# Optimization experiments

Measured on AMD Instinct MI355X. Metric: run time of the kernel, lower is better.

The kernel has to match this reference:

```python
import jax, jax.numpy as jnp
import numpy as np
import itertools
from functools import partial

H, W = 224, 448            # output raster size
R = 2                      # splat_radius
RADIUS_SCALE = 1.5
B, T, V, GH, GW = 1, 2, 2, 56, 112   # batch, time, views, gaussian grid
N = V * GH * GW            # gaussians per (b,t)
OFFSETS = jnp.array(list(itertools.product(range(-R, R + 1), repeat=2)), dtype=jnp.int32)  # (K,2)


def setup_inputs() -> dict:
    key = jax.random.key(0)
    ks = jax.random.split(key, 8)
    center = jax.random.normal(ks[0], (B, T, V, GH, GW, 3), jnp.float32) * 2.0
    scale = jax.random.uniform(ks[1], (B, T, V, GH, GW, 3), jnp.float32) * 0.1
    feat_dc = jax.random.uniform(ks[2], (B, T, V, GH, GW, 3), jnp.float32)
    opacity = jax.random.uniform(ks[3], (B, T, V, GH, GW, 1), jnp.float32)
    background_prob = jax.random.uniform(ks[4], (B, T, V, GH, GW), jnp.float32)
    sem_proj_2d = jax.random.uniform(ks[5], (B, T, V, 3, H, W), jnp.float32)
    # realistic pinhole intrinsics: fx=fy=220, principal point at image center
    camera_intrinsics = jnp.broadcast_to(jnp.array([220.0, 220.0, W / 2.0, H / 2.0], jnp.float32), (B, V, 4))
    # cameras ~5m behind the (origin-centered) point cloud, identity rotation + jittered translation
    trans = jnp.array([0.0, 0.0, -5.0], jnp.float32) + 0.2 * jax.random.normal(ks[6], (B, T, V, 3), jnp.float32)
    c2w = jnp.broadcast_to(jnp.eye(4, dtype=jnp.float32), (B, T, V, 4, 4))
    camera_to_world = c2w.at[..., :3, 3].set(trans)
    first_ego_pose_world = jnp.broadcast_to(jnp.eye(4, dtype=jnp.float32), (B, 4, 4))
    return {"center": center, "scale": scale, "feat_dc": feat_dc, "opacity": opacity,
            "background_prob": background_prob, "sem_proj_2d": sem_proj_2d,
            "camera_intrinsics": camera_intrinsics, "camera_to_world": camera_to_world,
            "first_ego_pose_world": first_ego_pose_world}


def _render_view(world, scale, color, alpha, intr, c2w):
    # world: (N,4) homogeneous world coords; scale,alpha: (N,); color: (N,3)
    fx, fy, cx, cy = intr[0], intr[1], intr[2], intr[3]
    w2c = jnp.linalg.inv(c2w)
    cam = (world @ w2c.T)[:, :3]              # (N,3) camera-frame coords
    z = cam[:, 2]
    finite = jnp.all(jnp.isfinite(cam), axis=-1)
    valid = (z > 1e-3) & finite & (alpha > 1e-5)
    z_safe = jnp.where(valid, z, 1.0)
    u = cam[:, 0] * fx / z_safe + cx
    v = cam[:, 1] * fy / z_safe + cy
    sigma = jnp.clip((fx + fy) * 0.5 * jnp.abs(scale) / jnp.maximum(z_safe, 1e-3), 0.75, 10.0)
    inb = (u >= -R - 1.0) & (u <= W + R) & (v >= -R - 1.0) & (v <= H + R)
    keep = valid & inb
    cnt = jnp.sum(keep)
    sigma_mean = jnp.where(cnt > 0, jnp.sum(jnp.where(keep, sigma, 0.0)) / jnp.maximum(cnt, 1), 0.0)
    a_eff = jnp.where(keep, alpha, 0.0)
    # depth sort front-to-back; dropped points carry zero alpha so their position is irrelevant
    order = jnp.argsort(jnp.where(keep, z, jnp.inf))
    u_s = jnp.where(keep, u, -1e6)[order]
    v_s = jnp.where(keep, v, -1e6)[order]
    sig_s = sigma[order]
    col_s = color[order]
    a_s = a_eff[order]
    x0 = jnp.floor(u_s).astype(jnp.int32)
    y0 = jnp.floor(v_s).astype(jnp.int32)
    radii = jnp.clip(jnp.ceil(sig_s * RADIUS_SCALE), 1, R).astype(jnp.int32)

    def step(carry, pt):
        alpha_den, rgb_num = carry
        x0p, y0p, up, vp, sp, ap, rp, colp = pt
        xo = x0p + OFFSETS[:, 0]
        yo = y0p + OFFSETS[:, 1]
        keep_off = ((jnp.abs(OFFSETS[:, 0]) <= rp) & (jnp.abs(OFFSETS[:, 1]) <= rp)
                    & (xo >= 0) & (xo < W) & (yo >= 0) & (yo < H))
        sp_c = jnp.maximum(sp, 1e-3)
        du = (up - xo.astype(up.dtype)) / sp_c
        dv = (vp - yo.astype(vp.dtype)) / sp_c
        la = jnp.clip(jnp.exp(-0.5 * (du * du + dv * dv)) * ap, 0.0, 0.999)
        idx = jnp.where(keep_off, yo * W + xo, H * W)   # OOB sentinel -> dropped by scatter
        old = alpha_den[jnp.clip(idx, 0, H * W - 1)]
        transmit = jnp.clip(1.0 - old, 0.0, 1.0)
        contrib = jnp.where(keep_off, la * transmit, 0.0)
        alpha_den = alpha_den.at[idx].set(jnp.clip(old + contrib, 0.0, 0.999), mode='drop')
        rgb_num = rgb_num.at[:, idx].add(colp[:, None] * contrib[None, :], mode='drop')
        return (alpha_den, rgb_num), None

    init = (jnp.zeros(H * W, jnp.float32), jnp.zeros((3, H * W), jnp.float32))
    (alpha_den, rgb_num), _ = jax.lax.scan(step, init, (x0, y0, u_s, v_s, sig_s, a_s, radii, col_s))
    touch = jnp.mean((alpha_den > 1e-6).astype(jnp.float32))
    rgb = jnp.clip(rgb_num, 0.0, 1.0).reshape(3, H, W)
    aout = jnp.clip(alpha_den, 0.0, 1.0).reshape(H, W)
    return rgb, aout, sigma_mean, touch


def _render_branch(centers, scales, colors, alpha, intr, c2w, first_pose):
    cf = centers.reshape(B, T, N, 3)
    sf = jnp.mean(scales, axis=-1).reshape(B, T, N)
    colf = jnp.clip(colors.reshape(B, T, N, 3), 0.0, 1.0)
    af = jnp.clip(alpha.reshape(B, T, N), 0.0, 1.0)
    xyz_h = jnp.concatenate([cf, jnp.ones((B, T, N, 1), cf.dtype)], axis=-1)
    world = jnp.einsum('bij,btnj->btni', first_pose, xyz_h)      # (B,T,N,4)
    M = B * T * V
    wv = jnp.broadcast_to(world[:, :, None], (B, T, V, N, 4)).reshape(M, N, 4)
    sv = jnp.broadcast_to(sf[:, :, None], (B, T, V, N)).reshape(M, N)
    cv = jnp.broadcast_to(colf[:, :, None], (B, T, V, N, 3)).reshape(M, N, 3)
    av = jnp.broadcast_to(af[:, :, None], (B, T, V, N)).reshape(M, N)
    iv = jnp.broadcast_to(intr[:, None], (B, T, V, 4)).reshape(M, 4)
    mv = c2w.reshape(M, 4, 4)
    rgb, aout, sm, tr = jax.vmap(_render_view)(wv, sv, cv, av, iv, mv)
    return (rgb.reshape(B, T, V, 3, H, W), aout.reshape(B, T, V, 1, H, W), jnp.mean(sm), jnp.mean(tr))


def reference(center, scale, feat_dc, opacity, background_prob, sem_proj_2d,
              camera_intrinsics, camera_to_world, first_ego_pose_world):
    base_alpha = jnp.clip(opacity[..., 0], 0.0, 1.0)                      # (B,T,V,GH,GW)
    dyn = jnp.clip(1.0 - background_prob.reshape(B, T, V, GH, GW), 0.0, 1.0)
    a_all = base_alpha
    a_dyn = base_alpha * dyn
    a_sta = base_alpha * (1.0 - dyn)
    rgb_all, al_all, sigma_mean, touch = _render_branch(center, scale, feat_dc, a_all, camera_intrinsics, camera_to_world, first_ego_pose_world)
    rgb_dyn, al_dyn, _, _ = _render_branch(center, scale, feat_dc, a_dyn, camera_intrinsics, camera_to_world, first_ego_pose_world)
    rgb_sta, al_sta, _, _ = _render_branch(center, scale, feat_dc, a_sta, camera_intrinsics, camera_to_world, first_ego_pose_world)
    return (rgb_sta, rgb_dyn, rgb_all, al_sta, al_dyn, al_all, sem_proj_2d, sigma_mean, touch)
```

## Files before the change

### kernel.cpp

```cpp
#include <hip/hip_runtime.h>
#include <cmath>

namespace {
constexpr int Hh = 224, Ww = 448;
constexpr int Tt = 2, Vv = 2, GH = 56, GW = 112;
constexpr int Nn = Vv * GH * GW;
constexpr int TV = Tt * Vv;
constexpr int TOT = TV * Nn;
constexpr int HW = Hh * Ww;
constexpr int TILE = 8;
constexpr int NTX = Ww / TILE;
constexpr int NTY = Hh / TILE;
constexpr int NTILES = TV * NTX * NTY;
constexpr int CAP_T = 256;

constexpr size_t RGB_SZ = (size_t)TV * 3 * HW;
constexpr size_t AL_SZ  = (size_t)TV * HW;
constexpr size_t OFF_RGB_STA = 0;
constexpr size_t OFF_RGB_DYN = RGB_SZ;
constexpr size_t OFF_RGB_ALL = 2 * RGB_SZ;
constexpr size_t OFF_AL_STA  = 3 * RGB_SZ;
constexpr size_t OFF_AL_DYN  = 3 * RGB_SZ + AL_SZ;
constexpr size_t OFF_AL_ALL  = 3 * RGB_SZ + 2 * AL_SZ;
constexpr size_t OFF_SEM     = 3 * RGB_SZ + 3 * AL_SZ;
constexpr size_t OFF_SM      = OFF_SEM + RGB_SZ;
constexpr size_t OFF_TOUCH   = OFF_SM + 1;

constexpr size_t WS_SUM  = (size_t)11 * TOT;
constexpr size_t WS_CNT  = WS_SUM + 4;
constexpr size_t WS_TCNT = WS_CNT + 4;
constexpr size_t WS_TPB  = WS_TCNT + NTILES;
constexpr size_t WS_LIST = WS_TPB + NTILES;
constexpr int    N_ZERO  = 8 + NTILES;
}

__device__ inline unsigned long long shfl_xor_u64(unsigned long long x, int m) {
  unsigned int lo = (unsigned int)x, hi = (unsigned int)(x >> 32);
  lo = __shfl_xor(lo, m, 64);
  hi = __shfl_xor(hi, m, 64);
  return ((unsigned long long)hi << 32) | lo;
}

__global__ __launch_bounds__(256) void init_k(const float4* __restrict__ sem,
                                              float4* __restrict__ dst,
                                              float* __restrict__ ws) {
  const int i = blockIdx.x * 256 + threadIdx.x;
  if (i < (int)(RGB_SZ / 4)) dst[i] = sem[i];
  if (blockIdx.x == gridDim.x - 1) {
    int* W = (int*)(ws + WS_SUM);
    for (int k = threadIdx.x; k < N_ZERO; k += 256) W[k] = 0;
  }
}

__global__ __launch_bounds__(256) void preprocess_k(
    const float* __restrict__ center, const float* __restrict__ scale,
    const float* __restrict__ feat, const float* __restrict__ opac,
    const float* __restrict__ bg, const float* __restrict__ intr,
    const float* __restrict__ fpose, const float* __restrict__ c2w,
    float* __restrict__ ws) {
#pragma clang fp contract(off)
  const int idx = blockIdx.x * 256 + threadIdx.x;
  const int n  = idx % Nn;
  const int tv = idx / Nn;
  const int v  = tv % Vv;
  const int t  = tv / Vv;
  const size_t gi = (size_t)t * Nn + n;

  float* Wz  = ws;
  float* Wu  = ws + (size_t)1 * TOT;
  float* Wvv = ws + (size_t)2 * TOT;
  float* Wsg = ws + (size_t)3 * TOT;
  int*   Wpk = (int*)(ws + (size_t)4 * TOT);
  float* Wr  = ws + (size_t)5 * TOT;
  float* Wg  = ws + (size_t)6 * TOT;
  float* Wb  = ws + (size_t)7 * TOT;
  float* Waa = ws + (size_t)8 * TOT;
  float* Wad = ws + (size_t)9 * TOT;
  float* Was = ws + (size_t)10 * TOT;
  float* Wsum = ws + WS_SUM;
  int*   Wcnt = (int*)(ws + WS_CNT);
  int*   Wtcnt = (int*)(ws + WS_TCNT);
  int*   Wlist = (int*)(ws + WS_LIST);

  double m00, m01, m02, m03, m10, m11, m12, m13,
         m20, m21, m22, m23, m30, m31, m32, m33;
  {
    const float* C = c2w + (size_t)tv * 16;
    m00 = C[0];  m01 = C[1];  m02 = C[2];  m03 = C[3];
    m10 = C[4];  m11 = C[5];  m12 = C[6];  m13 = C[7];
    m20 = C[8];  m21 = C[9];  m22 = C[10]; m23 = C[11];
    m30 = C[12]; m31 = C[13]; m32 = C[14]; m33 = C[15];
  }
  const double s0d = m00 * m11 - m10 * m01;
  const double s1d = m00 * m12 - m10 * m02;
  const double s2d = m00 * m13 - m10 * m03;
  const double s3d = m01 * m12 - m11 * m02;
  const double s4d = m01 * m13 - m11 * m03;
  const double s5d = m02 * m13 - m12 * m03;
  const double c5d = m22 * m33 - m32 * m23;
  const double c4d = m21 * m33 - m31 * m23;
  const double c3d = m21 * m32 - m31 * m22;
  const double c2d = m20 * m33 - m30 * m23;
  const double c1d = m20 * m32 - m30 * m22;
  const double c0d = m20 * m31 - m30 * m21;
  const double invdet =
      1.0 / (s0d * c5d - s1d * c4d + s2d * c3d + s3d * c2d - s4d * c1d + s5d * c0d);
  const float M0  = (float)(( m11 * c5d - m12 * c4d + m13 * c3d) * invdet);
  const float M1  = (float)((-m01 * c5d + m02 * c4d - m03 * c3d) * invdet);
  const float M2  = (float)(( m31 * s5d - m32 * s4d + m33 * s3d) * invdet);
  const float M3  = (float)((-m21 * s5d + m22 * s4d - m23 * s3d) * invdet);
  const float M4  = (float)((-m10 * c5d + m12 * c2d - m13 * c1d) * invdet);
  const float M5  = (float)(( m00 * c5d - m02 * c2d + m03 * c1d) * invdet);
  const float M6  = (float)((-m30 * s5d + m32 * s2d - m33 * s1d) * invdet);
  const float M7  = (float)(( m20 * s5d - m22 * s2d + m23 * s1d) * invdet);
  const float M8  = (float)(( m10 * c4d - m11 * c2d + m13 * c0d) * invdet);
  const float M9  = (float)((-m00 * c4d + m01 * c2d - m03 * c0d) * invdet);
  const float M10 = (float)(( m30 * s4d - m31 * s2d + m33 * s0d) * invdet);
  const float M11 = (float)((-m20 * s4d + m21 * s2d - m23 * s0d) * invdet);

  const float c0 = center[gi * 3 + 0], c1 = center[gi * 3 + 1], c2 = center[gi * 3 + 2];
  const float s0 = scale[gi * 3 + 0], s1 = scale[gi * 3 + 1], s2 = scale[gi * 3 + 2];
  const float sf = ((s0 + s1) + s2) / 3.0f;
  const float colr = fminf(fmaxf(feat[gi * 3 + 0], 0.0f), 1.0f);
  const float colg = fminf(fmaxf(feat[gi * 3 + 1], 0.0f), 1.0f);
  const float colb = fminf(fmaxf(feat[gi * 3 + 2], 0.0f), 1.0f);
  const float base = fminf(fmaxf(opac[gi], 0.0f), 1.0f);
  const float dyn  = fminf(fmaxf(1.0f - bg[gi], 0.0f), 1.0f);
  const float aAll = base;
  const float aDyn = base * dyn;
  const float aSta = base * (1.0f - dyn);

  float wd[4];
  for (int i = 0; i < 4; ++i)
    wd[i] = ((fpose[i * 4 + 0] * c0 + fpose[i * 4 + 1] * c1) + fpose[i * 4 + 2] * c2) +
            fpose[i * 4 + 3] * 1.0f;

  const float cam0 = ((M0 * wd[0] + M1 * wd[1]) + M2  * wd[2]) + M3  * wd[3];
  const float cam1 = ((M4 * wd[0] + M5 * wd[1]) + M6  * wd[2]) + M7  * wd[3];
  const float cam2 = ((M8 * wd[0] + M9 * wd[1]) + M10 * wd[2]) + M11 * wd[3];
  const bool fin = (fabsf(cam0) <= 3.4028235e38f) && (fabsf(cam1) <= 3.4028235e38f) &&
                   (fabsf(cam2) <= 3.4028235e38f);
  const float z = cam2;
  const float fx = intr[v * 4 + 0], fy = intr[v * 4 + 1];
  const float ppx = intr[v * 4 + 2], ppy = intr[v * 4 + 3];

  bool kept = false;
  float u = 0.0f, vv2 = 0.0f, sig = 0.0f;
  if ((z > 0.001f) && fin) {
    u   = cam0 * fx / z + ppx;
    vv2 = cam1 * fy / z + ppy;
    float tsc = (fx + fy) * 0.5f;
    sig = tsc * fabsf(sf);
    sig = sig / fmaxf(z, 0.001f);
    sig = fminf(fmaxf(sig, 0.75f), 10.0f);
    const bool inb = (u >= -3.0f) && (u <= 450.0f) && (vv2 >= -3.0f) && (vv2 <= 226.0f);
    kept = inb && (aAll > 1e-5f);
  }

  if (kept) {
    Wz[idx] = z; Wu[idx] = u; Wvv[idx] = vv2; Wsg[idx] = sig;
    const int x0 = (int)floorf(u);
    const int y0 = (int)floorf(vv2);
    const float rc = ceilf(sig * 1.5f);
    const int rad = rc < 1.0f ? 1 : (rc > 2.0f ? 2 : (int)rc);
    Wpk[idx] = ((x0 + 4) << 16) | ((y0 + 4) << 4) | rad;
    Wr[idx] = colr; Wg[idx] = colg; Wb[idx] = colb;
    Waa[idx] = aAll; Wad[idx] = aDyn; Was[idx] = aSta;
    const int x_lo = x0 - rad, x_hi = x0 + rad;
    const int y_lo = y0 - rad, y_hi = y0 + rad;
    if (x_hi >= 0 && x_lo < Ww && y_hi >= 0 && y_lo < Hh) {
      const int tx_lo = (x_lo > 0 ? x_lo : 0) >> 3;
      const int tx_hi = (x_hi < Ww - 1 ? x_hi : Ww - 1) >> 3;
      const int ty_lo = (y_lo > 0 ? y_lo : 0) >> 3;
      const int ty_hi = (y_hi < Hh - 1 ? y_hi : Hh - 1) >> 3;
      for (int ty = ty_lo; ty <= ty_hi; ++ty)
        for (int tx = tx_lo; tx <= tx_hi; ++tx) {
          const int tile = (tv * NTY + ty) * NTX + tx;
          const int slot = atomicAdd(&Wtcnt[tile], 1);
          if (slot < CAP_T) Wlist[(size_t)tile * CAP_T + slot] = n;
        }
    }
  }

  float sred = kept ? sig : 0.0f;
  int   cred = kept ? 1 : 0;
  #pragma unroll
  for (int off = 32; off > 0; off >>= 1) {
    sred += __shfl_down(sred, off, 64);
    cred += __shfl_down(cred, off, 64);
  }
  __shared__ float bsum[4];
  __shared__ int   bcnt[4];
  const int wv = threadIdx.x >> 6;
  if ((threadIdx.x & 63) == 0) { bsum[wv] = sred; bcnt[wv] = cred; }
  __syncthreads();
  if (threadIdx.x == 0) {
    const float ts = ((bsum[0] + bsum[1]) + bsum[2]) + bsum[3];
    const int   tc = bcnt[0] + bcnt[1] + bcnt[2] + bcnt[3];
    if (tc > 0) {
      atomicAdd(&Wsum[tv], ts);
      atomicAdd(&Wcnt[tv], tc);
    }
  }
}

__global__ __launch_bounds__(64) void raster_k(float* __restrict__ ws,
                                               float* __restrict__ out) {
#pragma clang fp contract(off)
  __shared__ unsigned long long s_key[CAP_T];
  __shared__ float s_u[64], s_v[64], s_sg[64];
  __shared__ float s_r[64], s_g[64], s_b[64];
  __shared__ float s_aa[64], s_ad[64], s_as[64];
  __shared__ int s_pk[64];

  const int tid = threadIdx.x;
  const int tv  = blockIdx.z;
  const int px  = blockIdx.x * TILE + (tid & 7);
  const int py  = blockIdx.y * TILE + (tid >> 3);
  const float fpx = (float)px, fpy = (float)py;
  const size_t base = (size_t)tv * Nn;

  const float* Wz  = ws;
  const float* Wu  = ws + (size_t)1 * TOT;
  const float* Wvv = ws + (size_t)2 * TOT;
  const float* Wsg = ws + (size_t)3 * TOT;
  const int*   Wpk = (const int*)(ws + (size_t)4 * TOT);
  const float* Wr  = ws + (size_t)5 * TOT;
  const float* Wg  = ws + (size_t)6 * TOT;
  const float* Wb  = ws + (size_t)7 * TOT;
  const float* Waa = ws + (size_t)8 * TOT;
  const float* Wad = ws + (size_t)9 * TOT;
  const float* Was = ws + (size_t)10 * TOT;
  int*       Wtpb  = (int*)(ws + WS_TPB);
  const int* Wtcnt = (const int*)(ws + WS_TCNT);
  const int* Wlist = (const int*)(ws + WS_LIST);

  const int tile = (tv * NTY + blockIdx.y) * NTX + blockIdx.x;
  const int cnt0 = Wtcnt[tile];
  const int cnt  = cnt0 < CAP_T ? cnt0 : CAP_T;
  const int* mylist = Wlist + (size_t)tile * CAP_T;

  float Aall = 0.0f, Adyn = 0.0f, Asta = 0.0f;
  float Ra = 0.0f, Ga = 0.0f, Ba = 0.0f;
  float Rd = 0.0f, Gd = 0.0f, Bd = 0.0f;
  float Rs = 0.0f, Gs = 0.0f, Bs = 0.0f;

  auto composite = [&](int m) {
    for (int j = 0; j < m; ++j) {
      const int pk  = s_pk[j];
      const int rad = pk & 15;
      const int y0  = ((pk >> 4) & 0xfff) - 4;
      const int x0  = (pk >> 16) - 4;
      if (abs(px - x0) <= rad && abs(py - y0) <= rad) {
        const float sg = s_sg[j];
        const float du = (s_u[j] - fpx) / sg;
        const float dv = (s_v[j] - fpy) / sg;
        const float gs = expf(-0.5f * (du * du + dv * dv));
        {
          const float la = fminf(fmaxf(gs * s_aa[j], 0.0f), 0.999f);
          const float tr = fminf(fmaxf(1.0f - Aall, 0.0f), 1.0f);
          const float ct = la * tr;
          Ra += s_r[j] * ct; Ga += s_g[j] * ct; Ba += s_b[j] * ct;
          Aall = fminf(fmaxf(Aall + ct, 0.0f), 0.999f);
        }
        const float ad = s_ad[j];
        if (ad > 1e-5f) {
          const float la = fminf(fmaxf(gs * ad, 0.0f), 0.999f);
          const float tr = fminf(fmaxf(1.0f - Adyn, 0.0f), 1.0f);
          const float ct = la * tr;
          Rd += s_r[j] * ct; Gd += s_g[j] * ct; Bd += s_b[j] * ct;
          Adyn = fminf(fmaxf(Adyn + ct, 0.0f), 0.999f);
        }
        const float as = s_as[j];
        if (as > 1e-5f) {
          const float la = fminf(fmaxf(gs * as, 0.0f), 0.999f);
          const float tr = fminf(fmaxf(1.0f - Asta, 0.0f), 1.0f);
          const float ct = la * tr;
          Rs += s_r[j] * ct; Gs += s_g[j] * ct; Bs += s_b[j] * ct;
          Asta = fminf(fmaxf(Asta + ct, 0.0f), 0.999f);
        }
      }
    }
  };

  if (cnt <= 64) {
    unsigned long long key = ~0ULL;
    if (tid < cnt) {
      const unsigned int n = (unsigned int)mylist[tid];
      key = ((unsigned long long)__float_as_uint(Wz[base + n]) << 32) | n;
    }
    if (cnt > 1) {
      for (int k = 2; k <= 64; k <<= 1) {
        for (int j = k >> 1; j > 0; j >>= 1) {
          const unsigned long long other = shfl_xor_u64(key, j);
          const bool up = ((tid & k) == 0);
          const bool keep_min = (up == ((tid & j) == 0));
          key = keep_min ? (key < other ? key : other) : (key > other ? key : other);
        }
      }
    }
    if (tid < cnt) {
      const int n = (int)(key & 0xffffffffULL);
      const size_t a = base + (size_t)n;
      s_u[tid] = Wu[a]; s_v[tid] = Wvv[a]; s_sg[tid] = Wsg[a]; s_pk[tid] = Wpk[a];
      s_r[tid] = Wr[a]; s_g[tid] = Wg[a]; s_b[tid] = Wb[a];
      s_aa[tid] = Waa[a]; s_ad[tid] = Wad[a]; s_as[tid] = Was[a];
    }
    __syncthreads();
    composite(cnt);
  } else {
    for (int i = tid; i < cnt; i += 64) {
      const unsigned int n = (unsigned int)mylist[i];
      s_key[i] = ((unsigned long long)__float_as_uint(Wz[base + n]) << 32) | n;
    }
    int P = 1;
    while (P < cnt) P <<= 1;
    for (int i = cnt + tid; i < P; i += 64) s_key[i] = ~0ULL;
    __syncthreads();
    for (int k = 2; k <= P; k <<= 1) {
      for (int j = k >> 1; j > 0; j >>= 1) {
        for (int i = tid; i < P; i += 64) {
          const int ixj = i ^ j;
          if (ixj > i) {
            const unsigned long long a = s_key[i], b2 = s_key[ixj];
            const bool up = ((i & k) == 0);
            if ((a > b2) == up) { s_key[i] = b2; s_key[ixj] = a; }
          }
        }
        __syncthreads();
      }
    }
    for (int cb = 0; cb < cnt; cb += 64) {
      const int m = min(64, cnt - cb);
      if (tid < m) {
        const int n = (int)(s_key[cb + tid] & 0xffffffffULL);
        const size_t a = base + (size_t)n;
        s_u[tid] = Wu[a]; s_v[tid] = Wvv[a]; s_sg[tid] = Wsg[a]; s_pk[tid] = Wpk[a];
        s_r[tid] = Wr[a]; s_g[tid] = Wg[a]; s_b[tid] = Wb[a];
        s_aa[tid] = Waa[a]; s_ad[tid] = Wad[a]; s_as[tid] = Was[a];
      }
      __syncthreads();
      composite(m);
      __syncthreads();
    }
  }

  const size_t pix = (size_t)py * Ww + px;
  const size_t hw  = (size_t)HW;
  const size_t m3  = (size_t)tv * 3;
  out[OFF_RGB_STA + (m3 + 0) * hw + pix] = fminf(fmaxf(Rs, 0.0f), 1.0f);
  out[OFF_RGB_STA + (m3 + 1) * hw + pix] = fminf(fmaxf(Gs, 0.0f), 1.0f);
  out[OFF_RGB_STA + (m3 + 2) * hw + pix] = fminf(fmaxf(Bs, 0.0f), 1.0f);
  out[OFF_RGB_DYN + (m3 + 0) * hw + pix] = fminf(fmaxf(Rd, 0.0f), 1.0f);
  out[OFF_RGB_DYN + (m3 + 1) * hw + pix] = fminf(fmaxf(Gd, 0.0f), 1.0f);
  out[OFF_RGB_DYN + (m3 + 2) * hw + pix] = fminf(fmaxf(Bd, 0.0f), 1.0f);
  out[OFF_RGB_ALL + (m3 + 0) * hw + pix] = fminf(fmaxf(Ra, 0.0f), 1.0f);
  out[OFF_RGB_ALL + (m3 + 1) * hw + pix] = fminf(fmaxf(Ga, 0.0f), 1.0f);
  out[OFF_RGB_ALL + (m3 + 2) * hw + pix] = fminf(fmaxf(Ba, 0.0f), 1.0f);
  out[OFF_AL_STA + (size_t)tv * hw + pix] = fminf(fmaxf(Asta, 0.0f), 1.0f);
  out[OFF_AL_DYN + (size_t)tv * hw + pix] = fminf(fmaxf(Adyn, 0.0f), 1.0f);
  out[OFF_AL_ALL + (size_t)tv * hw + pix] = fminf(fmaxf(Aall, 0.0f), 1.0f);

  const unsigned long long bal = __ballot(Aall > 1e-6f);
  if (tid == 0) Wtpb[tile] = (int)__popcll(bal);
}

__global__ __launch_bounds__(256) void finalize_k(const float* __restrict__ ws,
                                                  float* __restrict__ out) {
  const int tid = threadIdx.x;
  const int* Wtpb = (const int*)(ws + WS_TPB);
  int acc = 0;
  for (int i = tid; i < NTILES; i += 256) acc += Wtpb[i];
  #pragma unroll
  for (int off = 32; off > 0; off >>= 1) acc += __shfl_down(acc, off, 64);
  __shared__ int wsum[4];
  if ((tid & 63) == 0) wsum[tid >> 6] = acc;
  __syncthreads();
  if (tid == 0) {
    const int grand = wsum[0] + wsum[1] + wsum[2] + wsum[3];
    const float* Wsum = ws + WS_SUM;
    const int*   Wcnt = (const int*)(ws + WS_CNT);
    float sm = 0.0f;
    for (int i = 0; i < TV; ++i) {
      const int c = Wcnt[i];
      sm += (c > 0) ? (Wsum[i] / (float)(c > 1 ? c : 1)) : 0.0f;
    }
    out[OFF_SM]    = sm / (float)TV;
    out[OFF_TOUCH] = (float)grand / (float)(HW * TV);
  }
}

extern "C" void kernel_launch(void* const* d_in, const int* in_sizes, int n_in,
                              void* d_out, int out_size, void* d_ws, size_t ws_size,
                              hipStream_t stream) {
  const float* center = (const float*)d_in[0];
  const float* scale  = (const float*)d_in[1];
  const float* feat   = (const float*)d_in[2];
  const float* opac   = (const float*)d_in[3];
  const float* bg     = (const float*)d_in[4];
  const float* sem    = (const float*)d_in[5];
  const float* intr   = (const float*)d_in[6];
  const float* c2w    = (const float*)d_in[7];
  const float* fpose  = (const float*)d_in[8];
  float* out = (float*)d_out;
  float* ws  = (float*)d_ws;

  const int copy_blocks = (int)((RGB_SZ / 4 + 255) / 256) + 1;
  hipLaunchKernelGGL(init_k, dim3(copy_blocks), dim3(256), 0, stream,
                     (const float4*)sem, (float4*)(out + OFF_SEM), ws);
  hipLaunchKernelGGL(preprocess_k, dim3(TOT / 256), dim3(256), 0, stream,
                     center, scale, feat, opac, bg, intr, fpose, c2w, ws);
  hipLaunchKernelGGL(raster_k, dim3(NTX, NTY, TV), dim3(64), 0, stream, ws, out);
  hipLaunchKernelGGL(finalize_k, dim3(1), dim3(256), 0, stream, ws, out);
}
```

Before: 127.9 us.

## Pack gaussian attributes into float4, fuse init/preprocess cooperatively, fold finalize into raster

Moves the zeroing and semantic copy plus preprocessing into a single cooperative kernel with a grid-wide sync, and falls back to two launches if the cooperative launch fails. The finalize kernel is removed: the last raster block, found with an atomic ticket counter, computes the summary scalars. Per-gaussian attributes are packed into three float4 arrays so raster does vectorized gathers instead of eleven scalar loads. This cuts launch count and gather traffic, but adds a grid sync and global atomics to the critical path.

```diff
diff --git a/kernel.cpp b/kernel.cpp
--- a/kernel.cpp
+++ b/kernel.cpp
@@ -1,5 +1,8 @@
 #include <hip/hip_runtime.h>
+#include <hip/hip_cooperative_groups.h>
 #include <cmath>
+
+namespace cg = cooperative_groups;
 
 namespace {
 constexpr int Hh = 224, Ww = 448;
@@ -26,12 +29,16 @@
 constexpr size_t OFF_SM      = OFF_SEM + RGB_SZ;
 constexpr size_t OFF_TOUCH   = OFF_SM + 1;
 
-constexpr size_t WS_SUM  = (size_t)11 * TOT;
+constexpr size_t WS_QA   = 0;
+constexpr size_t WS_QB   = (size_t)4 * TOT;
+constexpr size_t WS_QC   = (size_t)8 * TOT;
+constexpr size_t WS_SUM  = (size_t)12 * TOT;
 constexpr size_t WS_CNT  = WS_SUM + 4;
-constexpr size_t WS_TCNT = WS_CNT + 4;
-constexpr size_t WS_TPB  = WS_TCNT + NTILES;
-constexpr size_t WS_LIST = WS_TPB + NTILES;
-constexpr int    N_ZERO  = 8 + NTILES;
+constexpr size_t WS_TOUCH  = WS_CNT + 4;
+constexpr size_t WS_TICKET = WS_TOUCH + 1;
+constexpr size_t WS_TCNT = WS_TICKET + 1;
+constexpr size_t WS_LIST = WS_TCNT + NTILES;
+constexpr int    N_ZERO  = 10 + NTILES;
 }
 
 __device__ inline unsigned long long shfl_xor_u64(unsigned long long x, int m) {
@@ -41,42 +48,30 @@
   return ((unsigned long long)hi << 32) | lo;
 }
 
-__global__ __launch_bounds__(256) void init_k(const float4* __restrict__ sem,
-                                              float4* __restrict__ dst,
-                                              float* __restrict__ ws) {
-  const int i = blockIdx.x * 256 + threadIdx.x;
-  if (i < (int)(RGB_SZ / 4)) dst[i] = sem[i];
-  if (blockIdx.x == gridDim.x - 1) {
-    int* W = (int*)(ws + WS_SUM);
-    for (int k = threadIdx.x; k < N_ZERO; k += 256) W[k] = 0;
-  }
-}
-
-__global__ __launch_bounds__(256) void preprocess_k(
+__device__ __forceinline__ void phaseA_body(const float4* __restrict__ sem,
+                                            float4* __restrict__ dst,
+                                            float* __restrict__ ws, int idx) {
+  int* Z = (int*)(ws + WS_SUM);
+  if (idx < N_ZERO) Z[idx] = 0;
+  for (int i = idx; i < (int)(RGB_SZ / 4); i += TOT) dst[i] = sem[i];
+}
+
+__device__ __forceinline__ void preprocess_body(
     const float* __restrict__ center, const float* __restrict__ scale,
     const float* __restrict__ feat, const float* __restrict__ opac,
     const float* __restrict__ bg, const float* __restrict__ intr,
     const float* __restrict__ fpose, const float* __restrict__ c2w,
-    float* __restrict__ ws) {
+    float* __restrict__ ws, int idx) {
 #pragma clang fp contract(off)
-  const int idx = blockIdx.x * 256 + threadIdx.x;
   const int n  = idx % Nn;
   const int tv = idx / Nn;
   const int v  = tv % Vv;
   const int t  = tv / Vv;
   const size_t gi = (size_t)t * Nn + n;
 
-  float* Wz  = ws;
-  float* Wu  = ws + (size_t)1 * TOT;
-  float* Wvv = ws + (size_t)2 * TOT;
-  float* Wsg = ws + (size_t)3 * TOT;
-  int*   Wpk = (int*)(ws + (size_t)4 * TOT);
-  float* Wr  = ws + (size_t)5 * TOT;
-  float* Wg  = ws + (size_t)6 * TOT;
-  float* Wb  = ws + (size_t)7 * TOT;
-  float* Waa = ws + (size_t)8 * TOT;
-  float* Wad = ws + (size_t)9 * TOT;
-  float* Was = ws + (size_t)10 * TOT;
+  float4* WqA = (float4*)(ws + WS_QA);
+  float4* WqB = (float4*)(ws + WS_QB);
+  float4* WqC = (float4*)(ws + WS_QC);
   float* Wsum = ws + WS_SUM;
   int*   Wcnt = (int*)(ws + WS_CNT);
   int*   Wtcnt = (int*)(ws + WS_TCNT);
@@ -158,14 +153,14 @@
   }
 
   if (kept) {
-    Wz[idx] = z; Wu[idx] = u; Wvv[idx] = vv2; Wsg[idx] = sig;
     const int x0 = (int)floorf(u);
     const int y0 = (int)floorf(vv2);
     const float rc = ceilf(sig * 1.5f);
     const int rad = rc < 1.0f ? 1 : (rc > 2.0f ? 2 : (int)rc);
-    Wpk[idx] = ((x0 + 4) << 16) | ((y0 + 4) << 4) | rad;
-    Wr[idx] = colr; Wg[idx] = colg; Wb[idx] = colb;
-    Waa[idx] = aAll; Wad[idx] = aDyn; Was[idx] = aSta;
+    const int pk = ((x0 + 4) << 16) | ((y0 + 4) << 4) | rad;
+    WqA[idx] = make_float4(z, u, vv2, sig);
+    WqB[idx] = make_float4(__int_as_float(pk), colr, colg, colb);
+    WqC[idx] = make_float4(aAll, aDyn, aSta, 0.0f);
     const int x_lo = x0 - rad, x_hi = x0 + rad;
     const int y_lo = y0 - rad, y_hi = y0 + rad;
     if (x_hi >= 0 && x_lo < Ww && y_hi >= 0 && y_lo < Hh) {
@@ -204,14 +199,41 @@
   }
 }
 
+__global__ __launch_bounds__(256) void prep_coop_k(
+    const float* __restrict__ center, const float* __restrict__ scale,
+    const float* __restrict__ feat, const float* __restrict__ opac,
+    const float* __restrict__ bg, const float* __restrict__ intr,
+    const float* __restrict__ fpose, const float* __restrict__ c2w,
+    float* __restrict__ ws, const float4* __restrict__ sem,
+    float4* __restrict__ semdst) {
+  const int idx = blockIdx.x * 256 + threadIdx.x;
+  phaseA_body(sem, semdst, ws, idx);
+  cg::this_grid().sync();
+  preprocess_body(center, scale, feat, opac, bg, intr, fpose, c2w, ws, idx);
+}
+
+__global__ __launch_bounds__(256) void init_k(const float4* __restrict__ sem,
+                                              float4* __restrict__ dst,
+                                              float* __restrict__ ws) {
+  const int idx = blockIdx.x * 256 + threadIdx.x;
+  phaseA_body(sem, dst, ws, idx);
+}
+
+__global__ __launch_bounds__(256) void prep_k(
+    const float* __restrict__ center, const float* __restrict__ scale,
+    const float* __restrict__ feat, const float* __restrict__ opac,
+    const float* __restrict__ bg, const float* __restrict__ intr,
+    const float* __restrict__ fpose, const float* __restrict__ c2w,
+    float* __restrict__ ws) {
+  const int idx = blockIdx.x * 256 + threadIdx.x;
+  preprocess_body(center, scale, feat, opac, bg, intr, fpose, c2w, ws, idx);
+}
+
 __global__ __launch_bounds__(64) void raster_k(float* __restrict__ ws,
                                                float* __restrict__ out) {
 #pragma clang fp contract(off)
   __shared__ unsigned long long s_key[CAP_T];
-  __shared__ float s_u[64], s_v[64], s_sg[64];
-  __shared__ float s_r[64], s_g[64], s_b[64];
-  __shared__ float s_aa[64], s_ad[64], s_as[64];
-  __shared__ int s_pk[64];
+  __shared__ float4 sA[64], sB[64], sC[64];
 
   const int tid = threadIdx.x;
   const int tv  = blockIdx.z;
@@ -220,18 +242,13 @@
   const float fpx = (float)px, fpy = (float)py;
   const size_t base = (size_t)tv * Nn;
 
-  const float* Wz  = ws;
-  const float* Wu  = ws + (size_t)1 * TOT;
-  const float* Wvv = ws + (size_t)2 * TOT;
-  const float* Wsg = ws + (size_t)3 * TOT;
-  const int*   Wpk = (const int*)(ws + (size_t)4 * TOT);
-  const float* Wr  = ws + (size_t)5 * TOT;
-  const float* Wg  = ws + (size_t)6 * TOT;
-  const float* Wb  = ws + (size_t)7 * TOT;
-  const float* Waa = ws + (size_t)8 * TOT;
-  const float* Wad = ws + (size_t)9 * TOT;
-  const float* Was = ws + (size_t)10 * TOT;
-  int*       Wtpb  = (int*)(ws + WS_TPB);
+  const float4* WqA = (const float4*)(ws + WS_QA);
+  const float4* WqB = (const float4*)(ws + WS_QB);
+  const float4* WqC = (const float4*)(ws + WS_QC);
+  const float* Wsum = ws + WS_SUM;
+  const int*   Wcnt = (const int*)(ws + WS_CNT);
+  int* Wtouch  = (int*)(ws + WS_TOUCH);
+  int* Wticket = (int*)(ws + WS_TICKET);
   const int* Wtcnt = (const int*)(ws + WS_TCNT);
   const int* Wlist = (const int*)(ws + WS_LIST);
 
@@ -247,36 +264,37 @@
 
   auto composite = [&](int m) {
     for (int j = 0; j < m; ++j) {
-      const int pk  = s_pk[j];
+      const float4 qb = sB[j];
+      const int pk  = __float_as_int(qb.x);
       const int rad = pk & 15;
       const int y0  = ((pk >> 4) & 0xfff) - 4;
       const int x0  = (pk >> 16) - 4;
       if (abs(px - x0) <= rad && abs(py - y0) <= rad) {
-        const float sg = s_sg[j];
-        const float du = (s_u[j] - fpx) / sg;
-        const float dv = (s_v[j] - fpy) / sg;
+        const float4 qa = sA[j];
+        const float sg = qa.w;
+        const float du = (qa.y - fpx) / sg;
+        const float dv = (qa.z - fpy) / sg;
         const float gs = expf(-0.5f * (du * du + dv * dv));
+        const float4 qc = sC[j];
         {
-          const float la = fminf(fmaxf(gs * s_aa[j], 0.0f), 0.999f);
+          const float la = fminf(fmaxf(gs * qc.x, 0.0f), 0.999f);
           const float tr = fminf(fmaxf(1.0f - Aall, 0.0f), 1.0f);
           const float ct = la * tr;
-          Ra += s_r[j] * ct; Ga += s_g[j] * ct; Ba += s_b[j] * ct;
+          Ra += qb.y * ct; Ga += qb.z * ct; Ba += qb.w * ct;
           Aall = fminf(fmaxf(Aall + ct, 0.0f), 0.999f);
         }
-        const float ad = s_ad[j];
-        if (ad > 1e-5f) {
-          const float la = fminf(fmaxf(gs * ad, 0.0f), 0.999f);
+        if (qc.y > 1e-5f) {
+          const float la = fminf(fmaxf(gs * qc.y, 0.0f), 0.999f);
           const float tr = fminf(fmaxf(1.0f - Adyn, 0.0f), 1.0f);
           const float ct = la * tr;
-          Rd += s_r[j] * ct; Gd += s_g[j] * ct; Bd += s_b[j] * ct;
+          Rd += qb.y * ct; Gd += qb.z * ct; Bd += qb.w * ct;
           Adyn = fminf(fmaxf(Adyn + ct, 0.0f), 0.999f);
         }
-        const float as = s_as[j];
-        if (as > 1e-5f) {
-          const float la = fminf(fmaxf(gs * as, 0.0f), 0.999f);
+        if (qc.z > 1e-5f) {
+          const float la = fminf(fmaxf(gs * qc.z, 0.0f), 0.999f);
           const float tr = fminf(fmaxf(1.0f - Asta, 0.0f), 1.0f);
           const float ct = la * tr;
-          Rs += s_r[j] * ct; Gs += s_g[j] * ct; Bs += s_b[j] * ct;
+          Rs += qb.y * ct; Gs += qb.z * ct; Bs += qb.w * ct;
           Asta = fminf(fmaxf(Asta + ct, 0.0f), 0.999f);
         }
       }
@@ -287,7 +305,8 @@
     unsigned long long key = ~0ULL;
     if (tid < cnt) {
       const unsigned int n = (unsigned int)mylist[tid];
-      key = ((unsigned long long)__float_as_uint(Wz[base + n]) << 32) | n;
+      const float z = ws[WS_QA + 4 * (base + (size_t)n)];
+      key = ((unsigned long long)__float_as_uint(z) << 32) | n;
     }
     if (cnt > 1) {
       for (int k = 2; k <= 64; k <<= 1) {
@@ -300,18 +319,16 @@
       }
     }
     if (tid < cnt) {
-      const int n = (int)(key & 0xffffffffULL);
-      const size_t a = base + (size_t)n;
-      s_u[tid] = Wu[a]; s_v[tid] = Wvv[a]; s_sg[tid] = Wsg[a]; s_pk[tid] = Wpk[a];
-      s_r[tid] = Wr[a]; s_g[tid] = Wg[a]; s_b[tid] = Wb[a];
-      s_aa[tid] = Waa[a]; s_ad[tid] = Wad[a]; s_as[tid] = Was[a];
+      const size_t a = base + (size_t)(int)(key & 0xffffffffULL);
+      sA[tid] = WqA[a]; sB[tid] = WqB[a]; sC[tid] = WqC[a];
     }
     __syncthreads();
     composite(cnt);
   } else {
     for (int i = tid; i < cnt; i += 64) {
       const unsigned int n = (unsigned int)mylist[i];
-      s_key[i] = ((unsigned long long)__float_as_uint(Wz[base + n]) << 32) | n;
+      const float z = ws[WS_QA + 4 * (base + (size_t)n)];
+      s_key[i] = ((unsigned long long)__float_as_uint(z) << 32) | n;
     }
     int P = 1;
     while (P < cnt) P <<= 1;
@@ -333,11 +350,8 @@
     for (int cb = 0; cb < cnt; cb += 64) {
       const int m = min(64, cnt - cb);
       if (tid < m) {
-        const int n = (int)(s_key[cb + tid] & 0xffffffffULL);
-        const size_t a = base + (size_t)n;
-        s_u[tid] = Wu[a]; s_v[tid] = Wvv[a]; s_sg[tid] = Wsg[a]; s_pk[tid] = Wpk[a];
-        s_r[tid] = Wr[a]; s_g[tid] = Wg[a]; s_b[tid] = Wb[a];
-        s_aa[tid] = Waa[a]; s_ad[tid] = Wad[a]; s_as[tid] = Was[a];
+        const size_t a = base + (size_t)(int)(s_key[cb + tid] & 0xffffffffULL);
+        sA[tid] = WqA[a]; sB[tid] = WqB[a]; sC[tid] = WqC[a];
       }
       __syncthreads();
       composite(m);
@@ -362,31 +376,21 @@
   out[OFF_AL_ALL + (size_t)tv * hw + pix] = fminf(fmaxf(Aall, 0.0f), 1.0f);
 
   const unsigned long long bal = __ballot(Aall > 1e-6f);
-  if (tid == 0) Wtpb[tile] = (int)__popcll(bal);
-}
-
-__global__ __launch_bounds__(256) void finalize_k(const float* __restrict__ ws,
-                                                  float* __restrict__ out) {
-  const int tid = threadIdx.x;
-  const int* Wtpb = (const int*)(ws + WS_TPB);
-  int acc = 0;
-  for (int i = tid; i < NTILES; i += 256) acc += Wtpb[i];
-  #pragma unroll
-  for (int off = 32; off > 0; off >>= 1) acc += __shfl_down(acc, off, 64);
-  __shared__ int wsum[4];
-  if ((tid & 63) == 0) wsum[tid >> 6] = acc;
-  __syncthreads();
   if (tid == 0) {
-    const int grand = wsum[0] + wsum[1] + wsum[2] + wsum[3];
-    const float* Wsum = ws + WS_SUM;
-    const int*   Wcnt = (const int*)(ws + WS_CNT);
-    float sm = 0.0f;
-    for (int i = 0; i < TV; ++i) {
-      const int c = Wcnt[i];
-      sm += (c > 0) ? (Wsum[i] / (float)(c > 1 ? c : 1)) : 0.0f;
-    }
-    out[OFF_SM]    = sm / (float)TV;
-    out[OFF_TOUCH] = (float)grand / (float)(HW * TV);
+    atomicAdd(Wtouch, (int)__popcll(bal));
+    __threadfence();
+    const int done = atomicAdd(Wticket, 1);
+    if (done == NTILES - 1) {
+      __threadfence();
+      float sm = 0.0f;
+      for (int i = 0; i < TV; ++i) {
+        const int c = Wcnt[i];
+        sm += (c > 0) ? (Wsum[i] / (float)(c > 1 ? c : 1)) : 0.0f;
+      }
+      const int grand = atomicAdd(Wtouch, 0);
+      out[OFF_SM]    = sm / (float)TV;
+      out[OFF_TOUCH] = (float)grand / (float)(HW * TV);
+    }
   }
 }
 
@@ -404,12 +408,21 @@
   const float* fpose  = (const float*)d_in[8];
   float* out = (float*)d_out;
   float* ws  = (float*)d_ws;
-
-  const int copy_blocks = (int)((RGB_SZ / 4 + 255) / 256) + 1;
-  hipLaunchKernelGGL(init_k, dim3(copy_blocks), dim3(256), 0, stream,
-                     (const float4*)sem, (float4*)(out + OFF_SEM), ws);
-  hipLaunchKernelGGL(preprocess_k, dim3(TOT / 256), dim3(256), 0, stream,
-                     center, scale, feat, opac, bg, intr, fpose, c2w, ws);
+  const float4* sem4 = (const float4*)sem;
+  float4* semdst = (float4*)(out + OFF_SEM);
+
+  void* args[] = {(void*)&center, (void*)&scale, (void*)&feat, (void*)&opac,
+                  (void*)&bg,     (void*)&intr,  (void*)&fpose, (void*)&c2w,
+                  (void*)&ws,     (void*)&sem4,  (void*)&semdst};
+  const hipError_t ce = hipLaunchCooperativeKernel(
+      reinterpret_cast<const void*>(&prep_coop_k), dim3(TOT / 256), dim3(256),
+      args, 0, stream);
+  if (ce != hipSuccess) {
+    (void)hipGetLastError();
+    hipLaunchKernelGGL(init_k, dim3(TOT / 256), dim3(256), 0, stream,
+                       sem4, semdst, ws);
+    hipLaunchKernelGGL(prep_k, dim3(TOT / 256), dim3(256), 0, stream,
+                       center, scale, feat, opac, bg, intr, fpose, c2w, ws);
+  }
   hipLaunchKernelGGL(raster_k, dim3(NTX, NTY, TV), dim3(64), 0, stream, ws, out);
-  hipLaunchKernelGGL(finalize_k, dim3(1), dim3(256), 0, stream, ws, out);
-}
+}
```

After: 354.9 us. +177.5%, slower.
